# Kernel tuning notes

Hardware: AMD Instinct MI355X
Metric: run time of the kernel (lower is better)

## Reference

```python
import jax, jax.numpy as jnp
import numpy as np

N_NODES = 100000
N_EDGES = 2000000
H = 128


def setup_inputs() -> dict:
    key = jax.random.key(0)
    ks = jax.random.split(key, 5)
    z_src = jax.random.normal(ks[0], (N_NODES, H), dtype=jnp.float32)
    z_dst = jax.random.normal(ks[1], (N_NODES, H), dtype=jnp.float32)
    edge_label_index = jax.random.randint(ks[2], (2, N_EDGES), 0, N_NODES, dtype=jnp.int64)
    # Linear(2H, H) and Linear(H, 1) params (stored as [in, out] for x @ W)
    W1 = jax.random.normal(ks[3], (2 * H, H), dtype=jnp.float32) * (1.0 / np.sqrt(2 * H))
    b1 = jnp.zeros((H,), dtype=jnp.float32)
    W2 = jax.random.normal(ks[4], (H, 1), dtype=jnp.float32) * (1.0 / np.sqrt(H))
    b2 = jnp.zeros((1,), dtype=jnp.float32)
    return {"z_src": z_src, "z_dst": z_dst, "edge_label_index": edge_label_index,
            "W1": W1, "b1": b1, "W2": W2, "b2": b2}


def reference(z_src, z_dst, edge_label_index, W1, b1, W2, b2):
    row, col = edge_label_index[0], edge_label_index[1]
    # gather + concat -> [E, 2H]
    z = jnp.concatenate([z_src[row], z_dst[col]], axis=-1)
    h = jax.nn.relu(z @ W1 + b1)          # [E, H]
    out = h @ W2 + b2                     # [E, 1]
    return out.reshape(-1)
```

## Files before the change

kernel.cpp:

```cpp
#include <hip/hip_runtime.h>

#define HDIM 128

typedef __bf16 bf16_t;
typedef bf16_t bf16x8 __attribute__((ext_vector_type(8)));
typedef float  f32x4  __attribute__((ext_vector_type(4)));

__device__ __forceinline__ unsigned short f2bf_rne(float f) {
    unsigned int u = __float_as_uint(f);
    u += 0x7fffu + ((u >> 16) & 1u);
    return (unsigned short)(u >> 16);
}
__device__ __forceinline__ unsigned int pk_bf2(float a, float b) {
    return (unsigned int)f2bf_rne(a) | ((unsigned int)f2bf_rne(b) << 16);
}

__global__ __launch_bounds__(256) void convert_w1(
    const float* __restrict__ W1, unsigned short* __restrict__ Wt)
{
    const int o = blockIdx.x * 256 + threadIdx.x;
    const int g = o >> 14, rem = o & 16383, n = rem >> 7, k = rem & 127;
    Wt[o] = f2bf_rne(W1[g * 16384 + k * 128 + n]);
}

#define ZP 136
__global__ __launch_bounds__(256) void node_gemm_mfma(
    const float* __restrict__ Zs, const float* __restrict__ Zd,
    const unsigned short* __restrict__ Wt, const float* __restrict__ b1,
    unsigned short* __restrict__ Abuf, unsigned short* __restrict__ Bbuf,
    int M, int gb)
{
    __shared__ unsigned short zs[64 * ZP];
    __shared__ unsigned short wsm[128 * ZP];

    const bool second = (blockIdx.x >= gb);
    const float* __restrict__ Z          = second ? Zd : Zs;
    const unsigned short* __restrict__ W = Wt + (second ? 128 * 128 : 0);
    unsigned short* __restrict__ C       = second ? Bbuf : Abuf;
    const int bx   = second ? (blockIdx.x - gb) : blockIdx.x;
    const int row0 = bx * 64;
    const int t    = threadIdx.x;

    #pragma unroll
    for (int j = 0; j < 8; ++j) {
        const int u   = t + 256 * j;
        const int row = u >> 5;
        const int c4  = u & 31;
        int rg = row0 + row; if (rg >= M) rg = M - 1;
        const float4 v = *reinterpret_cast<const float4*>(Z + (size_t)rg * HDIM + c4 * 4);
        uint2 p; p.x = pk_bf2(v.x, v.y); p.y = pk_bf2(v.z, v.w);
        *reinterpret_cast<uint2*>(zs + row * ZP + c4 * 4) = p;
    }
    #pragma unroll
    for (int j = 0; j < 8; ++j) {
        const int u  = t + 256 * j;
        const int n  = u >> 4;
        const int k8 = u & 15;
        const uint4 v = *reinterpret_cast<const uint4*>(W + n * 128 + k8 * 8);
        *reinterpret_cast<uint4*>(wsm + n * ZP + k8 * 8) = v;
    }
    __syncthreads();

    const int lane = t & 63;
    const int wave = t >> 6;
    const int m    = lane & 15;
    const int quad = lane >> 4;
    const int rw   = wave & 1;
    const int cw   = wave >> 1;

    const int aoff0 = (rw * 32 +  0 + m) * ZP + quad * 8;
    const int aoff1 = (rw * 32 + 16 + m) * ZP + quad * 8;
    const int boff  = (cw * 64 + m) * ZP + quad * 8;

    f32x4 acc[2][4] = {};
    #pragma unroll
    for (int ks = 0; ks < 4; ++ks) {
        const int ko = ks * 32;
        const bf16x8 a0 = *reinterpret_cast<const bf16x8*>(zs + aoff0 + ko);
        const bf16x8 a1 = *reinterpret_cast<const bf16x8*>(zs + aoff1 + ko);
        #pragma unroll
        for (int ct = 0; ct < 4; ++ct) {
            const bf16x8 bb = *reinterpret_cast<const bf16x8*>(wsm + boff + ct * 16 * ZP + ko);
            acc[0][ct] = __builtin_amdgcn_mfma_f32_16x16x32_bf16(a0, bb, acc[0][ct], 0, 0, 0);
            acc[1][ct] = __builtin_amdgcn_mfma_f32_16x16x32_bf16(a1, bb, acc[1][ct], 0, 0, 0);
        }
    }

    const int colbase = cw * 64 + m;
    #pragma unroll
    for (int ct = 0; ct < 4; ++ct) {
        const int col = colbase + ct * 16;
        const float bv = second ? b1[col] : 0.f;
        #pragma unroll
        for (int rt = 0; rt < 2; ++rt) {
            #pragma unroll
            for (int i = 0; i < 4; ++i) {
                const int gr = row0 + rw * 32 + rt * 16 + quad * 4 + i;
                if (gr < M)
                    C[(size_t)gr * HDIM + col] = f2bf_rne(acc[rt][ct][i] + bv);
            }
        }
    }
}

__global__ __launch_bounds__(256) void edge_decode_bf16(
    const unsigned short* __restrict__ A, const unsigned short* __restrict__ Bm,
    const int* __restrict__ idx,
    const float* __restrict__ W2, const float* __restrict__ b2,
    float* __restrict__ out, int E)
{
    const int t   = threadIdx.x;
    const int sub = t & 15;
    const int grp = t >> 4;

    float w2r[8];
    #pragma unroll
    for (int i = 0; i < 8; ++i) w2r[i] = W2[sub * 8 + i];
    const float b2s = b2[0];

    const int G = gridDim.x * 16;
    for (int e0 = blockIdx.x * 16 + grp; e0 < E; e0 += 2 * G) {
        const int  e1 = e0 + G;
        const bool h1 = (e1 < E);
        const int r0 = idx[e0];
        const int c0 = idx[E + e0];
        const int r1 = h1 ? idx[e1]     : r0;
        const int c1 = h1 ? idx[E + e1] : c0;

        const uint4 a0 = *reinterpret_cast<const uint4*>(A  + (size_t)r0 * HDIM + sub * 8);
        const uint4 b0 = *reinterpret_cast<const uint4*>(Bm + (size_t)c0 * HDIM + sub * 8);
        const uint4 a1 = *reinterpret_cast<const uint4*>(A  + (size_t)r1 * HDIM + sub * 8);
        const uint4 b1v = *reinterpret_cast<const uint4*>(Bm + (size_t)c1 * HDIM + sub * 8);

        float s0 = 0.f, s1 = 0.f;
        #pragma unroll
        for (int i = 0; i < 4; ++i) {
            unsigned int ua = (&a0.x)[i], ub = (&b0.x)[i];
            s0 += fmaxf(__uint_as_float(ua << 16)        + __uint_as_float(ub << 16),        0.f) * w2r[2 * i];
            s0 += fmaxf(__uint_as_float(ua & 0xffff0000u) + __uint_as_float(ub & 0xffff0000u), 0.f) * w2r[2 * i + 1];
            unsigned int uc = (&a1.x)[i], ud = (&b1v.x)[i];
            s1 += fmaxf(__uint_as_float(uc << 16)        + __uint_as_float(ud << 16),        0.f) * w2r[2 * i];
            s1 += fmaxf(__uint_as_float(uc & 0xffff0000u) + __uint_as_float(ud & 0xffff0000u), 0.f) * w2r[2 * i + 1];
        }
        #pragma unroll
        for (int d = 1; d < 16; d <<= 1) {
            s0 += __shfl_xor(s0, d);
            s1 += __shfl_xor(s1, d);
        }
        if (sub == 0) {
            out[e0] = s0 + b2s;
            if (h1) out[e1] = s1 + b2s;
        }
    }
}

extern "C" void kernel_launch(void* const* d_in, const int* in_sizes, int n_in,
                              void* d_out, int out_size, void* d_ws, size_t ws_size,
                              hipStream_t stream)
{
    const float* z_src = (const float*)d_in[0];
    const float* z_dst = (const float*)d_in[1];
    const int*   eidx  = (const int*)d_in[2];
    const float* W1    = (const float*)d_in[3];
    const float* b1    = (const float*)d_in[4];
    const float* W2    = (const float*)d_in[5];
    const float* b2    = (const float*)d_in[6];
    float*       outp  = (float*)d_out;

    const int Nn = in_sizes[0] / HDIM;
    const int E  = in_sizes[2] / 2;

    unsigned short* Abuf = (unsigned short*)d_ws;
    unsigned short* Bbuf = Abuf + (size_t)Nn * HDIM;
    unsigned short* Wt   = Bbuf + (size_t)Nn * HDIM;

    convert_w1<<<128, 256, 0, stream>>>(W1, Wt);

    const int gb = (Nn + 63) / 64;
    node_gemm_mfma<<<2 * gb, 256, 0, stream>>>(z_src, z_dst, Wt, b1, Abuf, Bbuf, Nn, gb);

    edge_decode_bf16<<<8192, 256, 0, stream>>>(Abuf, Bbuf, eidx, W2, b2, outp, E);
}
```

Before: 296.3 us.

## Stream W1 fragments from global in node GEMM and simplify edge loop

The node GEMM no longer stages the bf16 W1 tile in shared memory. Each wave keeps its 16-row Z fragment in registers and reads W fragments directly from global memory, relying on L2/L1 hits, and swaps MFMA operands so each lane writes four contiguous output columns as packed stores. The edge decode loop drops the two-edges-per-iteration unroll in favour of one edge per iteration, which lowers register use but leaves fewer gathers in flight per thread. Shared memory use and sync work fall, at the cost of repeated global reads of W per block and less memory-level parallelism in the edge kernel.

```diff
diff --git a/kernel.cpp b/kernel.cpp
--- a/kernel.cpp
+++ b/kernel.cpp
@@ -31,7 +31,6 @@
     int M, int gb)
 {
     __shared__ unsigned short zs[64 * ZP];
-    __shared__ unsigned short wsm[128 * ZP];
 
     const bool second = (blockIdx.x >= gb);
     const float* __restrict__ Z          = second ? Zd : Zs;
@@ -51,54 +50,44 @@
         uint2 p; p.x = pk_bf2(v.x, v.y); p.y = pk_bf2(v.z, v.w);
         *reinterpret_cast<uint2*>(zs + row * ZP + c4 * 4) = p;
     }
-    #pragma unroll
-    for (int j = 0; j < 8; ++j) {
-        const int u  = t + 256 * j;
-        const int n  = u >> 4;
-        const int k8 = u & 15;
-        const uint4 v = *reinterpret_cast<const uint4*>(W + n * 128 + k8 * 8);
-        *reinterpret_cast<uint4*>(wsm + n * ZP + k8 * 8) = v;
-    }
     __syncthreads();
 
     const int lane = t & 63;
     const int wave = t >> 6;
     const int m    = lane & 15;
     const int quad = lane >> 4;
-    const int rw   = wave & 1;
-    const int cw   = wave >> 1;
 
-    const int aoff0 = (rw * 32 +  0 + m) * ZP + quad * 8;
-    const int aoff1 = (rw * 32 + 16 + m) * ZP + quad * 8;
-    const int boff  = (cw * 64 + m) * ZP + quad * 8;
+    bf16x8 zf[4];
+    {
+        const unsigned short* zp = zs + (wave * 16 + m) * ZP + quad * 8;
+        #pragma unroll
+        for (int ks = 0; ks < 4; ++ks)
+            zf[ks] = *reinterpret_cast<const bf16x8*>(zp + ks * 32);
+    }
 
-    f32x4 acc[2][4] = {};
+    f32x4 acc[8] = {};
     #pragma unroll
-    for (int ks = 0; ks < 4; ++ks) {
-        const int ko = ks * 32;
-        const bf16x8 a0 = *reinterpret_cast<const bf16x8*>(zs + aoff0 + ko);
-        const bf16x8 a1 = *reinterpret_cast<const bf16x8*>(zs + aoff1 + ko);
+    for (int ct = 0; ct < 8; ++ct) {
+        const unsigned short* wp = W + (ct * 16 + m) * HDIM + quad * 8;
         #pragma unroll
-        for (int ct = 0; ct < 4; ++ct) {
-            const bf16x8 bb = *reinterpret_cast<const bf16x8*>(wsm + boff + ct * 16 * ZP + ko);
-            acc[0][ct] = __builtin_amdgcn_mfma_f32_16x16x32_bf16(a0, bb, acc[0][ct], 0, 0, 0);
-            acc[1][ct] = __builtin_amdgcn_mfma_f32_16x16x32_bf16(a1, bb, acc[1][ct], 0, 0, 0);
+        for (int ks = 0; ks < 4; ++ks) {
+            const bf16x8 wf = *reinterpret_cast<const bf16x8*>(wp + ks * 32);
+            acc[ct] = __builtin_amdgcn_mfma_f32_16x16x32_bf16(wf, zf[ks], acc[ct], 0, 0, 0);
         }
     }
 
-    const int colbase = cw * 64 + m;
-    #pragma unroll
-    for (int ct = 0; ct < 4; ++ct) {
-        const int col = colbase + ct * 16;
-        const float bv = second ? b1[col] : 0.f;
+    const int grow = row0 + wave * 16 + m;
+    if (grow < M) {
+        unsigned short* crow = C + (size_t)grow * HDIM;
         #pragma unroll
-        for (int rt = 0; rt < 2; ++rt) {
-            #pragma unroll
-            for (int i = 0; i < 4; ++i) {
-                const int gr = row0 + rw * 32 + rt * 16 + quad * 4 + i;
-                if (gr < M)
-                    C[(size_t)gr * HDIM + col] = f2bf_rne(acc[rt][ct][i] + bv);
-            }
+        for (int ct = 0; ct < 8; ++ct) {
+            const int col = ct * 16 + quad * 4;
+            float4 bv = make_float4(0.f, 0.f, 0.f, 0.f);
+            if (second) bv = *reinterpret_cast<const float4*>(b1 + col);
+            uint2 o;
+            o.x = pk_bf2(acc[ct][0] + bv.x, acc[ct][1] + bv.y);
+            o.y = pk_bf2(acc[ct][2] + bv.z, acc[ct][3] + bv.w);
+            *reinterpret_cast<uint2*>(crow + col) = o;
         }
     }
 }
@@ -118,39 +107,26 @@
     for (int i = 0; i < 8; ++i) w2r[i] = W2[sub * 8 + i];
     const float b2s = b2[0];
 
-    const int G = gridDim.x * 16;
-    for (int e0 = blockIdx.x * 16 + grp; e0 < E; e0 += 2 * G) {
-        const int  e1 = e0 + G;
-        const bool h1 = (e1 < E);
-        const int r0 = idx[e0];
-        const int c0 = idx[E + e0];
-        const int r1 = h1 ? idx[e1]     : r0;
-        const int c1 = h1 ? idx[E + e1] : c0;
+    const int stride = gridDim.x * 16;
+    for (int e = blockIdx.x * 16 + grp; e < E; e += stride) {
+        const int r = idx[e];
+        const int c = idx[E + e];
+        const uint4 av = *reinterpret_cast<const uint4*>(A  + (size_t)r * HDIM + sub * 8);
+        const uint4 bv = *reinterpret_cast<const uint4*>(Bm + (size_t)c * HDIM + sub * 8);
 
-        const uint4 a0 = *reinterpret_cast<const uint4*>(A  + (size_t)r0 * HDIM + sub * 8);
-        const uint4 b0 = *reinterpret_cast<const uint4*>(Bm + (size_t)c0 * HDIM + sub * 8);
-        const uint4 a1 = *reinterpret_cast<const uint4*>(A  + (size_t)r1 * HDIM + sub * 8);
-        const uint4 b1v = *reinterpret_cast<const uint4*>(Bm + (size_t)c1 * HDIM + sub * 8);
-
-        float s0 = 0.f, s1 = 0.f;
+        float s = 0.f;
         #pragma unroll
         for (int i = 0; i < 4; ++i) {
-            unsigned int ua = (&a0.x)[i], ub = (&b0.x)[i];
-            s0 += fmaxf(__uint_as_float(ua << 16)        + __uint_as_float(ub << 16),        0.f) * w2r[2 * i];
-            s0 += fmaxf(__uint_as_float(ua & 0xffff0000u) + __uint_as_float(ub & 0xffff0000u), 0.f) * w2r[2 * i + 1];
-            unsigned int uc = (&a1.x)[i], ud = (&b1v.x)[i];
-            s1 += fmaxf(__uint_as_float(uc << 16)        + __uint_as_float(ud << 16),        0.f) * w2r[2 * i];
-            s1 += fmaxf(__uint_as_float(uc & 0xffff0000u) + __uint_as_float(ud & 0xffff0000u), 0.f) * w2r[2 * i + 1];
+            const unsigned int ua = (&av.x)[i];
+            const unsigned int ub = (&bv.x)[i];
+            s += fmaxf(__uint_as_float(ua << 16)         + __uint_as_float(ub << 16),         0.f) * w2r[2 * i];
+            s += fmaxf(__uint_as_float(ua & 0xffff0000u) + __uint_as_float(ub & 0xffff0000u), 0.f) * w2r[2 * i + 1];
         }
-        #pragma unroll
-        for (int d = 1; d < 16; d <<= 1) {
-            s0 += __shfl_xor(s0, d);
-            s1 += __shfl_xor(s1, d);
-        }
-        if (sub == 0) {
-            out[e0] = s0 + b2s;
-            if (h1) out[e1] = s1 + b2s;
-        }
+        s += __shfl_xor(s, 1);
+        s += __shfl_xor(s, 2);
+        s += __shfl_xor(s, 4);
+        s += __shfl_xor(s, 8);
+        if (sub == 0) out[e] = s + b2s;
     }
 }
 
```

Result: slower. 329.6 us (+11.2%).
